# Kernel tuning notes

Measured on AMD Instinct MI355X. Metric: run time of the kernel, lower is better.

Reference implementation:

```python
import jax, jax.numpy as jnp
import numpy as np

B, M, N = 16, 128, 256
USER_DIM, ANT_DIM, EDGE_DIM = 8, 2, 1
HIDDEN, HEADS = 128, 4
HD = HIDDEN // HEADS
WB, DMIN, HZ, PMAX = 2.0, 0.01, 10.0, 1.0
SCALE = 1.0 / float(np.sqrt(HD))
NEG = 0.2  # leaky relu slope


def leaky(x):
    return jnp.where(x >= 0, x, NEG * x)


def ln(x, g, b, eps=1e-5):
    m = jnp.mean(x, axis=-1, keepdims=True)
    v = jnp.mean((x - m) ** 2, axis=-1, keepdims=True)
    return (x - m) * jax.lax.rsqrt(v + eps) * g + b


def setup_inputs() -> dict:
    key = jax.random.key(0)
    ks = jax.random.split(key, 16)
    rn = lambda k, shape, s: jax.random.normal(k, shape, jnp.float32) * s
    inp = {
        "user_feats": jax.random.normal(ks[0], (B, M, USER_DIM), jnp.float32),
        "ant_feats": jax.random.uniform(ks[1], (B, N, ANT_DIM), jnp.float32),
        "edge_feats": jax.random.uniform(ks[2], (B, M, N, EDGE_DIM), jnp.float32),
        # per-head projections (Linear no-bias) + their LayerNorm affine params
        "Wu": rn(ks[3], (HEADS, HD, USER_DIM), 0.5),
        "ln_u_g": jnp.ones((HEADS, HD)), "ln_u_b": jnp.zeros((HEADS, HD)),
        "Wa": rn(ks[4], (HEADS, HD, ANT_DIM), 0.5),
        "ln_a_g": jnp.ones((HEADS, HD)), "ln_a_b": jnp.zeros((HEADS, HD)),
        "We": rn(ks[5], (HEADS, HD, EDGE_DIM), 0.5),
        "ln_e_g": jnp.ones((HEADS, HD)), "ln_e_b": jnp.zeros((HEADS, HD)),
        "attn_v": rn(ks[6], (HEADS, HD), 0.5),
        # residual proj for antennas (the user residual branch is dead code in the block)
        "Wra": rn(ks[7], (HIDDEN, ANT_DIM), 0.5), "bra": jnp.zeros((HIDDEN,)),
        "ln_ant_g": jnp.ones((HIDDEN,)), "ln_ant_b": jnp.zeros((HIDDEN,)),
        # mlp_ant
        "Wm1": rn(ks[8], (HIDDEN // 2, HIDDEN), 0.1), "bm1": jnp.full((HIDDEN // 2,), 0.1),
        "Wm2": rn(ks[9], (2, HIDDEN // 2), 0.1), "bm2": jnp.full((2,), 0.1),
        # readouts over antenna axis
        "Wd1": rn(ks[10], (2 * N, N), 0.05), "bd1": jnp.zeros((2 * N,)),
        "Wd2": rn(ks[11], (N, 2 * N), 0.05), "bd2": jnp.zeros((N,)),
        "Wp1": rn(ks[12], (2 * N, N), 0.05), "bp1": jnp.zeros((2 * N,)),
        "Wp2": rn(ks[13], (N, 2 * N), 0.05), "bp2": jnp.zeros((N,)),
    }
    return inp


def reference(user_feats, ant_feats, edge_feats, Wu, ln_u_g, ln_u_b, Wa, ln_a_g, ln_a_b,
              We, ln_e_g, ln_e_b, attn_v, Wra, bra, ln_ant_g, ln_ant_b,
              Wm1, bm1, Wm2, bm2, Wd1, bd1, Wd2, bd2, Wp1, bp1, Wp2, bp2):
    # --- per-head bipartite attention (all heads batched on axis h) ---
    U = leaky(ln(jnp.einsum('bmi,hdi->hbmd', user_feats, Wu), ln_u_g[:, None, None, :], ln_u_b[:, None, None, :]))  # [h,B,M,hd]
    A = leaky(ln(jnp.einsum('bni,hdi->hbnd', ant_feats, Wa), ln_a_g[:, None, None, :], ln_a_b[:, None, None, :]))   # [h,B,N,hd]
    E = leaky(ln(jnp.einsum('bmni,hdi->hbmnd', edge_feats, We), ln_e_g[:, None, None, None, :], ln_e_b[:, None, None, None, :]))  # [h,B,M,N,hd]
    inter = leaky(U[:, :, :, None, :] + A[:, :, None, :, :] + E)                # [h,B,M,N,hd]
    scores = jnp.einsum('hbmnd,hd->hbmn', inter, attn_v) * SCALE
    alpha = jax.nn.softmax(scores, axis=-1)                                      # max-subtract softmax over N
    ant_out = jnp.einsum('hbmd,hbmn->hbnd', U, alpha)                            # [h,B,N,hd]
    ant_cat = jnp.transpose(ant_out, (1, 2, 0, 3)).reshape(B, N, HIDDEN)         # concat heads
    a_attn = jax.nn.relu(ant_cat + leaky(ant_feats @ Wra.T + bra))
    # --- block readouts ---
    a_attn = ln(a_attn, ln_ant_g, ln_ant_b)
    h1 = jax.nn.relu(a_attn @ Wm1.T + bm1)
    ant2d = jnp.clip(jax.nn.relu(h1 @ Wm2.T + bm2), -200.0, 200.0)               # [B,N,2]
    rd = jax.nn.relu(ant2d[..., 0] @ Wd1.T + bd1) @ Wd2.T + bd2                  # [B,N]
    rp = jax.nn.relu(ant2d[..., 1] @ Wp1.T + bp1) @ Wp2.T + bp2                  # [B,N]
    rd = jnp.clip(rd, 0.0, 100.0)
    rp = jnp.nan_to_num(rp, nan=0.0, posinf=1.0, neginf=0.0)
    # delta path
    Bmax = 2.0 * WB - (N - 1) * DMIN
    da = jax.nn.relu(rd)
    sd = jnp.sum(da, axis=1, keepdims=True)
    sdelta = jnp.clip((Bmax / jnp.maximum(Bmax, sd)) * da, 0.0, 100.0)
    idx = jnp.arange(N, dtype=sdelta.dtype)
    # closed form of the sequential recurrence x[n] = x[n-1] + sdelta[n] + DMIN - WB
    x = jnp.cumsum(sdelta, axis=1) + idx * DMIN - (idx + 1.0) * WB
    positions = jnp.stack([x, jnp.zeros_like(x), jnp.full_like(x, HZ)], axis=-1)  # [B,N,3]
    # power path
    eps = 1e-3
    pa = jnp.clip(jnp.nan_to_num(jax.nn.relu(rp), nan=0.0, posinf=1.0, neginf=0.0), 0.0, 1.0)
    sp = jnp.nan_to_num(jnp.sum(pa, axis=1, keepdims=True), nan=eps, posinf=eps, neginf=-eps)
    denom = jnp.maximum(sp, eps)
    sfp = jax.lax.stop_gradient(jnp.nan_to_num(PMAX / denom, nan=1.0, posinf=1.0, neginf=0.0))
    spow = jnp.clip(jnp.nan_to_num(sfp * pa, nan=0.0, posinf=1.0, neginf=0.0), 0.0, 1.0)
    ant_feats_out = jnp.stack([sdelta, spow], axis=-1)                            # [B,N,2]
    diff = user_feats[..., :2][:, :, None, :] - positions[:, None, :, :2]         # [B,M,N,2]
    edge_feats_new = jnp.sqrt(jnp.sum(diff * diff, axis=-1, keepdims=True))       # [B,M,N,1]
    return (ant_feats_out, edge_feats_new, positions)
```

## Files before the change

### kernel.cpp

```cpp
#include <hip/hip_runtime.h>
#include <math.h>

#define H_   4
#define HD_  32
#define B_   16
#define M_   128
#define N_   256
#define MC_  8
#define MCH_ 16
#define SCALE_ 0.17677669529663687f

__device__ __forceinline__ float lrelu_f(float x) { return x >= 0.f ? x : 0.2f * x; }

__global__ __launch_bounds__(256) void k2_attn(
    const float* __restrict__ uf, const float* __restrict__ af,
    const float* __restrict__ edge,
    const float* __restrict__ Wu, const float* __restrict__ gu, const float* __restrict__ bu,
    const float* __restrict__ Wa, const float* __restrict__ ga, const float* __restrict__ ba,
    const float* __restrict__ We, const float* __restrict__ ge, const float* __restrict__ be,
    const float* __restrict__ av, float* __restrict__ P)
{
  int blk = blockIdx.x;
  int h = blk & 3, b = (blk >> 2) & 15, mc = blk >> 6;
  int tid = threadIdx.x, n = tid;
  int lane = tid & 63, wid = tid >> 6;
  __shared__ float AB[N_ * 33];
  __shared__ float4 Ut4[HD_][4];
  __shared__ float4 cbv[HD_];
  __shared__ float wred[2][MCH_][4];
  __shared__ float vw_s;

  if (tid < 32) {
    int d = tid;
    float w = We[h * HD_ + d];
    float s = w;
    #pragma unroll
    for (int o = 16; o > 0; o >>= 1) s += __shfl_xor(s, o, 32);
    float mw = s * (1.f / 32.f);
    float df = w - mw;
    float v2 = df * df;
    #pragma unroll
    for (int o = 16; o > 0; o >>= 1) v2 += __shfl_xor(v2, o, 32);
    if (d == 0) vw_s = v2 * (1.f / 32.f);
    float vv = av[h * HD_ + d] * SCALE_;
    cbv[d] = make_float4(df * ge[h * HD_ + d], be[h * HD_ + d], 0.6f * vv, 0.4f * vv);
  }
  int m0 = mc * MCH_;
  {
    int m_loc = tid >> 4, s = tid & 15, dd = s * 2;
    const float* urow = uf + (size_t)(b * M_ + m0 + m_loc) * 8;
    const float* w0 = Wu + (h * HD_ + dd) * 8;
    float x0 = 0.f, x1 = 0.f;
    #pragma unroll
    for (int i = 0; i < 8; ++i) { float u = urow[i]; x0 = fmaf(u, w0[i], x0); x1 = fmaf(u, w0[8 + i], x1); }
    float sm = x0 + x1;
    #pragma unroll
    for (int o = 8; o > 0; o >>= 1) sm += __shfl_xor(sm, o, 64);
    float mean = sm * (1.f / 32.f);
    float d0 = x0 - mean, d1 = x1 - mean;
    float vv = fmaf(d0, d0, d1 * d1);
    #pragma unroll
    for (int o = 8; o > 0; o >>= 1) vv += __shfl_xor(vv, o, 64);
    float rs = rsqrtf(vv * (1.f / 32.f) + 1e-5f);
    float y0 = fmaf(d0 * rs, gu[h * HD_ + dd],     bu[h * HD_ + dd]);
    float y1 = fmaf(d1 * rs, gu[h * HD_ + dd + 1], bu[h * HD_ + dd + 1]);
    ((float*)Ut4)[dd * 16 + m_loc]       = lrelu_f(y0);
    ((float*)Ut4)[(dd + 1) * 16 + m_loc] = lrelu_f(y1);
  }
  {
    float a0 = af[(b * N_ + n) * 2 + 0], a1 = af[(b * N_ + n) * 2 + 1];
    float ar[HD_]; float sm = 0.f;
    #pragma unroll
    for (int d = 0; d < HD_; ++d) {
      ar[d] = fmaf(a0, Wa[(h * HD_ + d) * 2], a1 * Wa[(h * HD_ + d) * 2 + 1]);
      sm += ar[d];
    }
    float mean = sm * (1.f / 32.f); float vv = 0.f;
    #pragma unroll
    for (int d = 0; d < HD_; ++d) { ar[d] -= mean; vv = fmaf(ar[d], ar[d], vv); }
    float rs = rsqrtf(vv * (1.f / 32.f) + 1e-5f);
    #pragma unroll
    for (int d = 0; d < HD_; ++d)
      AB[n * 33 + d] = lrelu_f(fmaf(ar[d] * rs, ga[h * HD_ + d], ba[h * HD_ + d]));
  }
  __syncthreads();
  float vw = vw_s;
  float tm[MCH_];
  #pragma unroll
  for (int mm = 0; mm < MCH_; ++mm) {
    float e = edge[(size_t)(b * M_ + m0 + mm) * N_ + n];
    tm[mm] = e * rsqrtf(fmaf(e * e, vw, 1e-5f));
  }
  float sc[MCH_];
  #pragma unroll
  for (int mm = 0; mm < MCH_; ++mm) sc[mm] = 0.f;
  const float* arow = &AB[n * 33];
  for (int d = 0; d < HD_; ++d) {
    float ad = arow[d];
    float4 qc = cbv[d];
    float4 u0 = Ut4[d][0], u1 = Ut4[d][1], u2 = Ut4[d][2], u3 = Ut4[d][3];
#define STEP(mi, uval) { float w_ = fmaf(tm[mi], qc.x, qc.y); \
    float E_ = fmaf(0.4f, fabsf(w_), 0.6f * w_); \
    float x_ = ad + uval + E_; \
    sc[mi] = fmaf(qc.z, x_, fmaf(qc.w, fabsf(x_), sc[mi])); }
    STEP(0, u0.x)  STEP(1, u0.y)  STEP(2, u0.z)  STEP(3, u0.w)
    STEP(4, u1.x)  STEP(5, u1.y)  STEP(6, u1.z)  STEP(7, u1.w)
    STEP(8, u2.x)  STEP(9, u2.y)  STEP(10, u2.z) STEP(11, u2.w)
    STEP(12, u3.x) STEP(13, u3.y) STEP(14, u3.z) STEP(15, u3.w)
#undef STEP
  }
  #pragma unroll
  for (int mm = 0; mm < MCH_; ++mm) {
    float v = sc[mm];
    #pragma unroll
    for (int o = 32; o > 0; o >>= 1) v = fmaxf(v, __shfl_xor(v, o, 64));
    if (lane == 0) wred[0][mm][wid] = v;
  }
  __syncthreads();
  #pragma unroll
  for (int mm = 0; mm < MCH_; ++mm) {
    float mx = fmaxf(fmaxf(wred[0][mm][0], wred[0][mm][1]),
                     fmaxf(wred[0][mm][2], wred[0][mm][3]));
    float em = __expf(sc[mm] - mx);
    sc[mm] = em;
    float ss = em;
    #pragma unroll
    for (int o = 32; o > 0; o >>= 1) ss += __shfl_xor(ss, o, 64);
    if (lane == 0) wred[1][mm][wid] = ss;
  }
  __syncthreads();
  #pragma unroll
  for (int mm = 0; mm < MCH_; ++mm) {
    float tot = (wred[1][mm][0] + wred[1][mm][1]) + (wred[1][mm][2] + wred[1][mm][3]);
    sc[mm] = sc[mm] / tot;
  }
  __syncthreads();
  float* accr = &AB[n * 33];
  for (int d = 0; d < HD_; ++d) {
    float4 u0 = Ut4[d][0], u1 = Ut4[d][1], u2 = Ut4[d][2], u3 = Ut4[d][3];
    float a0 = 0.f;
    a0 = fmaf(sc[0], u0.x, a0);  a0 = fmaf(sc[1], u0.y, a0);
    a0 = fmaf(sc[2], u0.z, a0);  a0 = fmaf(sc[3], u0.w, a0);
    a0 = fmaf(sc[4], u1.x, a0);  a0 = fmaf(sc[5], u1.y, a0);
    a0 = fmaf(sc[6], u1.z, a0);  a0 = fmaf(sc[7], u1.w, a0);
    a0 = fmaf(sc[8], u2.x, a0);  a0 = fmaf(sc[9], u2.y, a0);
    a0 = fmaf(sc[10], u2.z, a0); a0 = fmaf(sc[11], u2.w, a0);
    a0 = fmaf(sc[12], u3.x, a0); a0 = fmaf(sc[13], u3.y, a0);
    a0 = fmaf(sc[14], u3.z, a0); a0 = fmaf(sc[15], u3.w, a0);
    accr[d] = a0;
  }
  __syncthreads();
  float* Pbase = P + (size_t)((mc * 4 + h) * B_ + b) * (N_ * HD_);
  for (int i = tid; i < N_ * HD_; i += 256) {
    int nn = i >> 5, d = i & 31;
    Pbase[i] = AB[nn * 33 + d];
  }
}

__global__ __launch_bounds__(256) void k3_mlp(
    const float* __restrict__ P, const float* __restrict__ af,
    const float* __restrict__ Wra, const float* __restrict__ bra,
    const float* __restrict__ gant, const float* __restrict__ bant,
    const float* __restrict__ Wm1, const float* __restrict__ bm1,
    const float* __restrict__ Wm2, const float* __restrict__ bm2,
    float* __restrict__ rd_in, float* __restrict__ rp_in)
{
  int b = blockIdx.x >> 4, nt = blockIdx.x & 15;
  int tid = threadIdx.x;
  int n_loc = tid >> 4, s = tid & 15;
  int n = nt * 16 + n_loc;
  int jj0 = s * 8;
  int hh = s >> 2, d0 = (s & 3) * 8;
  __shared__ float Wm1s[64][128];
  __shared__ float a2s[16][128];
  __shared__ float h1s[16][64];

  {
    const float4* wg = (const float4*)Wm1;
    float4* wl = (float4*)Wm1s;
    #pragma unroll
    for (int k = 0; k < 8; ++k) wl[tid + 256 * k] = wg[tid + 256 * k];
  }
  float cat[8];
  #pragma unroll
  for (int k = 0; k < 8; ++k) cat[k] = 0.f;
  #pragma unroll
  for (int mc = 0; mc < MC_; ++mc) {
    const float* base = P + (size_t)((mc * 4 + hh) * B_ + b) * (N_ * HD_) + n * HD_ + d0;
    float4 p0 = ((const float4*)base)[0], p1 = ((const float4*)base)[1];
    cat[0] += p0.x; cat[1] += p0.y; cat[2] += p0.z; cat[3] += p0.w;
    cat[4] += p1.x; cat[5] += p1.y; cat[6] += p1.z; cat[7] += p1.w;
  }
  float af0 = af[(b * N_ + n) * 2 + 0], af1 = af[(b * N_ + n) * 2 + 1];
  float a1[8]; float sm = 0.f;
  #pragma unroll
  for (int k = 0; k < 8; ++k) {
    int jj = jj0 + k;
    float r = fmaf(Wra[jj * 2], af0, fmaf(Wra[jj * 2 + 1], af1, bra[jj]));
    a1[k] = fmaxf(cat[k] + lrelu_f(r), 0.f);
    sm += a1[k];
  }
  #pragma unroll
  for (int o = 8; o > 0; o >>= 1) sm += __shfl_xor(sm, o, 64);
  float mean = sm * (1.f / 128.f);
  float vv = 0.f;
  #pragma unroll
  for (int k = 0; k < 8; ++k) { a1[k] -= mean; vv = fmaf(a1[k], a1[k], vv); }
  #pragma unroll
  for (int o = 8; o > 0; o >>= 1) vv += __shfl_xor(vv, o, 64);
  float rs = rsqrtf(vv * (1.f / 128.f) + 1e-5f);
  #pragma unroll
  for (int k = 0; k < 8; ++k) {
    int jj = jj0 + k;
    a2s[n_loc][jj] = fmaf(a1[k] * rs, gant[jj], bant[jj]);
  }
  __syncthreads();
  #pragma unroll
  for (int k = 0; k < 4; ++k) {
    int o = tid + 256 * k;
    int row = o & 63, nl = o >> 6;
    const float4* wr = (const float4*)Wm1s[row];
    const float4* xr = (const float4*)a2s[nl];
    float c0 = 0.f, c1 = 0.f, c2 = 0.f, c3 = 0.f;
    #pragma unroll
    for (int c = 0; c < 32; ++c) {
      int cc = (c + row) & 31;
      float4 w = wr[cc], x = xr[cc];
      c0 = fmaf(w.x, x.x, c0); c1 = fmaf(w.y, x.y, c1);
      c2 = fmaf(w.z, x.z, c2); c3 = fmaf(w.w, x.w, c3);
    }
    h1s[nl][row] = fmaxf((c0 + c1) + (c2 + c3) + bm1[row], 0.f);
  }
  __syncthreads();
  {
    int c = s >> 3, e0 = (s & 7) * 8;
    float p = 0.f;
    #pragma unroll
    for (int k = 0; k < 8; ++k) p = fmaf(h1s[n_loc][e0 + k], Wm2[c * 64 + e0 + k], p);
    #pragma unroll
    for (int o = 4; o > 0; o >>= 1) p += __shfl_xor(p, o, 64);
    if ((s & 7) == 0) {
      float v = p + bm2[c];
      v = fminf(fmaxf(v, 0.f), 200.f);
      (c == 0 ? rd_in : rp_in)[b * N_ + n] = v;
    }
  }
}

__global__ __launch_bounds__(256) void k4a_l1(
    const float* __restrict__ rd_in, const float* __restrict__ rp_in,
    const float* __restrict__ Wd1, const float* __restrict__ bd1,
    const float* __restrict__ Wp1, const float* __restrict__ bp1,
    float* __restrict__ d1buf)
{
  int r = blockIdx.x * 4 + (threadIdx.x >> 6);
  int lane = threadIdx.x & 63;
  int path = r >> 13;
  int rem = r & 8191;
  int b = rem >> 9, i = rem & 511;
  const float* W = (path ? Wp1 : Wd1) + (size_t)i * N_;
  const float* bias = path ? bp1 : bd1;
  const float* x = (path ? rp_in : rd_in) + b * N_;
  float4 w = ((const float4*)W)[lane];
  float4 xv = ((const float4*)x)[lane];
  float s = fmaf(w.x, xv.x, fmaf(w.y, xv.y, fmaf(w.z, xv.z, w.w * xv.w)));
  #pragma unroll
  for (int o = 32; o > 0; o >>= 1) s += __shfl_xor(s, o, 64);
  if (lane == 0) d1buf[r] = fmaxf(s + bias[i], 0.f);
}

__global__ __launch_bounds__(256) void k4b_l2(
    const float* __restrict__ d1buf,
    const float* __restrict__ Wd2, const float* __restrict__ bd2,
    const float* __restrict__ Wp2, const float* __restrict__ bp2,
    float* __restrict__ rdbuf, float* __restrict__ rpbuf)
{
  int r = blockIdx.x * 4 + (threadIdx.x >> 6);
  int lane = threadIdx.x & 63;
  int path = r >> 12;
  int rem = r & 4095;
  int b = rem >> 8, n = rem & 255;
  const float* W = (path ? Wp2 : Wd2) + (size_t)n * (2 * N_);
  const float* x = d1buf + path * (B_ * 2 * N_) + b * (2 * N_);
  float4 w0 = ((const float4*)W)[lane * 2], w1 = ((const float4*)W)[lane * 2 + 1];
  float4 x0 = ((const float4*)x)[lane * 2], x1 = ((const float4*)x)[lane * 2 + 1];
  float s = fmaf(w0.x, x0.x, fmaf(w0.y, x0.y, fmaf(w0.z, x0.z, w0.w * x0.w)));
  s = fmaf(w1.x, x1.x, fmaf(w1.y, x1.y, fmaf(w1.z, x1.z, fmaf(w1.w, x1.w, s))));
  #pragma unroll
  for (int o = 32; o > 0; o >>= 1) s += __shfl_xor(s, o, 64);
  if (lane == 0) {
    if (path == 0) {
      float rd = s + bd2[n];
      rd = fminf(fmaxf(rd, 0.f), 100.f);
      rdbuf[b * N_ + n] = rd;
    } else {
      float rp = s + bp2[n];
      if (isnan(rp)) rp = 0.f;
      else if (isinf(rp)) rp = rp > 0.f ? 1.f : 0.f;
      float pa = fminf(fmaxf(rp, 0.f), 1.f);
      rpbuf[b * N_ + n] = pa;
    }
  }
}

__global__ __launch_bounds__(256) void k4c_final(
    const float* __restrict__ rdbuf, const float* __restrict__ rpbuf,
    const float* __restrict__ uf,
    float* __restrict__ out_af, float* __restrict__ out_pos, float* __restrict__ out_edge)
{
  int b = blockIdx.x >> 4, g = blockIdx.x & 15;
  int q = threadIdx.x;
  int lane = q & 63, wid = q >> 6;
  __shared__ float red[8];
  float rd = rdbuf[b * N_ + q];
  float pa = rpbuf[b * N_ + q];
  float s = rd, s2 = pa;
  #pragma unroll
  for (int o = 32; o > 0; o >>= 1) { s += __shfl_xor(s, o, 64); s2 += __shfl_xor(s2, o, 64); }
  if (lane == 0) { red[wid] = s; red[4 + wid] = s2; }
  __syncthreads();
  float sd = red[0] + red[1] + red[2] + red[3];
  float sp = red[4] + red[5] + red[6] + red[7];
  const float Bmax = 2.f * 2.0f - (N_ - 1) * 0.01f;
  float f = Bmax / fmaxf(Bmax, sd);
  float sdelta = fminf(fmaxf(f * rd, 0.f), 100.f);
  float sfp = 1.0f / fmaxf(sp, 1e-3f);
  float spow = fminf(sfp * pa, 1.f);
  float val = sdelta;
  #pragma unroll
  for (int o = 1; o < 64; o <<= 1) {
    float t = __shfl_up(val, o, 64);
    if (lane >= o) val += t;
  }
  __syncthreads();
  if (lane == 63) red[wid] = val;
  __syncthreads();
  float off = 0.f;
  #pragma unroll
  for (int w2 = 0; w2 < 4; ++w2) if (w2 < wid) off += red[w2];
  float x = val + off + (float)q * 0.01f - (float)(q + 1) * 2.0f;
  if (g == 0) {
    out_af[(b * N_ + q) * 2 + 0] = sdelta;
    out_af[(b * N_ + q) * 2 + 1] = spow;
    out_pos[(b * N_ + q) * 3 + 0] = x;
    out_pos[(b * N_ + q) * 3 + 1] = 0.f;
    out_pos[(b * N_ + q) * 3 + 2] = 10.0f;
  }
  #pragma unroll
  for (int k = 0; k < 8; ++k) {
    int m = g * 8 + k;
    float u0 = uf[(b * M_ + m) * 8 + 0], u1 = uf[(b * M_ + m) * 8 + 1];
    float dx = u0 - x;
    out_edge[(size_t)(b * M_ + m) * N_ + q] = sqrtf(fmaf(dx, dx, u1 * u1));
  }
}

extern "C" void kernel_launch(void* const* d_in, const int* in_sizes, int n_in,
                              void* d_out, int out_size, void* d_ws, size_t ws_size,
                              hipStream_t stream) {
  (void)in_sizes; (void)n_in; (void)out_size; (void)ws_size;
  const float* uf   = (const float*)d_in[0];
  const float* af   = (const float*)d_in[1];
  const float* edge = (const float*)d_in[2];
  const float* Wu   = (const float*)d_in[3];
  const float* gu   = (const float*)d_in[4];
  const float* bu   = (const float*)d_in[5];
  const float* Wa   = (const float*)d_in[6];
  const float* ga   = (const float*)d_in[7];
  const float* ba   = (const float*)d_in[8];
  const float* We   = (const float*)d_in[9];
  const float* ge   = (const float*)d_in[10];
  const float* be   = (const float*)d_in[11];
  const float* av   = (const float*)d_in[12];
  const float* Wra  = (const float*)d_in[13];
  const float* bra  = (const float*)d_in[14];
  const float* gant = (const float*)d_in[15];
  const float* bant = (const float*)d_in[16];
  const float* Wm1  = (const float*)d_in[17];
  const float* bm1  = (const float*)d_in[18];
  const float* Wm2  = (const float*)d_in[19];
  const float* bm2  = (const float*)d_in[20];
  const float* Wd1  = (const float*)d_in[21];
  const float* bd1  = (const float*)d_in[22];
  const float* Wd2  = (const float*)d_in[23];
  const float* bd2  = (const float*)d_in[24];
  const float* Wp1  = (const float*)d_in[25];
  const float* bp1  = (const float*)d_in[26];
  const float* Wp2  = (const float*)d_in[27];
  const float* bp2  = (const float*)d_in[28];

  float* ws    = (float*)d_ws;
  float* P     = ws;
  float* rd_in = ws + 4194304;
  float* rp_in = ws + 4198400;
  float* d1buf = ws + 4202496;
  float* rdbuf = ws + 4218880;
  float* rpbuf = ws + 4222976;

  float* out      = (float*)d_out;
  float* out_af   = out;
  float* out_edge = out + 8192;
  float* out_pos  = out + 532480;

  hipLaunchKernelGGL(k2_attn, dim3(512), dim3(256), 0, stream,
                     uf, af, edge, Wu, gu, bu, Wa, ga, ba, We, ge, be, av, P);
  hipLaunchKernelGGL(k3_mlp, dim3(256), dim3(256), 0, stream,
                     P, af, Wra, bra, gant, bant, Wm1, bm1, Wm2, bm2, rd_in, rp_in);
  hipLaunchKernelGGL(k4a_l1, dim3(4096), dim3(256), 0, stream,
                     rd_in, rp_in, Wd1, bd1, Wp1, bp1, d1buf);
  hipLaunchKernelGGL(k4b_l2, dim3(2048), dim3(256), 0, stream,
                     d1buf, Wd2, bd2, Wp2, bp2, rdbuf, rpbuf);
  hipLaunchKernelGGL(k4c_final, dim3(256), dim3(256), 0, stream,
                     rdbuf, rpbuf, uf, out_af, out_pos, out_edge);
}
```

Measured before the change: 167.8 us.

## Split attention into 16 user chunks and keep antenna features in registers

Halves the per-block user chunk from 16 to 8 and doubles the attention grid to 1024 blocks. The launch bound now asks for 4 blocks per CU, aiming for more waves in flight. Each thread's antenna feature vector stays in registers instead of a shared-memory row, which removes one barrier. The cost is twice as many partial-output tiles, so the P workspace doubles and the MLP kernel must read and reduce twice as many partials.

```diff
diff --git a/kernel.cpp b/kernel.cpp
--- a/kernel.cpp
+++ b/kernel.cpp
@@ -6,13 +6,13 @@
 #define B_   16
 #define M_   128
 #define N_   256
-#define MC_  8
-#define MCH_ 16
+#define MC_  16
+#define MCH_ 8
 #define SCALE_ 0.17677669529663687f
 
 __device__ __forceinline__ float lrelu_f(float x) { return x >= 0.f ? x : 0.2f * x; }
 
-__global__ __launch_bounds__(256) void k2_attn(
+__global__ __launch_bounds__(256, 4) void k2_attn(
     const float* __restrict__ uf, const float* __restrict__ af,
     const float* __restrict__ edge,
     const float* __restrict__ Wu, const float* __restrict__ gu, const float* __restrict__ bu,
@@ -25,7 +25,7 @@
   int tid = threadIdx.x, n = tid;
   int lane = tid & 63, wid = tid >> 6;
   __shared__ float AB[N_ * 33];
-  __shared__ float4 Ut4[HD_][4];
+  __shared__ float4 Ut4[HD_][2];
   __shared__ float4 cbv[HD_];
   __shared__ float wred[2][MCH_][4];
   __shared__ float vw_s;
@@ -46,7 +46,7 @@
     cbv[d] = make_float4(df * ge[h * HD_ + d], be[h * HD_ + d], 0.6f * vv, 0.4f * vv);
   }
   int m0 = mc * MCH_;
-  {
+  if (tid < 128) {
     int m_loc = tid >> 4, s = tid & 15, dd = s * 2;
     const float* urow = uf + (size_t)(b * M_ + m0 + m_loc) * 8;
     const float* w0 = Wu + (h * HD_ + dd) * 8;
@@ -64,12 +64,13 @@
     float rs = rsqrtf(vv * (1.f / 32.f) + 1e-5f);
     float y0 = fmaf(d0 * rs, gu[h * HD_ + dd],     bu[h * HD_ + dd]);
     float y1 = fmaf(d1 * rs, gu[h * HD_ + dd + 1], bu[h * HD_ + dd + 1]);
-    ((float*)Ut4)[dd * 16 + m_loc]       = lrelu_f(y0);
-    ((float*)Ut4)[(dd + 1) * 16 + m_loc] = lrelu_f(y1);
-  }
+    ((float*)Ut4)[dd * MCH_ + m_loc]       = lrelu_f(y0);
+    ((float*)Ut4)[(dd + 1) * MCH_ + m_loc] = lrelu_f(y1);
+  }
+  float ar[HD_];
   {
     float a0 = af[(b * N_ + n) * 2 + 0], a1 = af[(b * N_ + n) * 2 + 1];
-    float ar[HD_]; float sm = 0.f;
+    float sm = 0.f;
     #pragma unroll
     for (int d = 0; d < HD_; ++d) {
       ar[d] = fmaf(a0, Wa[(h * HD_ + d) * 2], a1 * Wa[(h * HD_ + d) * 2 + 1]);
@@ -81,7 +82,7 @@
     float rs = rsqrtf(vv * (1.f / 32.f) + 1e-5f);
     #pragma unroll
     for (int d = 0; d < HD_; ++d)
-      AB[n * 33 + d] = lrelu_f(fmaf(ar[d] * rs, ga[h * HD_ + d], ba[h * HD_ + d]));
+      ar[d] = lrelu_f(fmaf(ar[d] * rs, ga[h * HD_ + d], ba[h * HD_ + d]));
   }
   __syncthreads();
   float vw = vw_s;
@@ -94,19 +95,17 @@
   float sc[MCH_];
   #pragma unroll
   for (int mm = 0; mm < MCH_; ++mm) sc[mm] = 0.f;
-  const float* arow = &AB[n * 33];
+  #pragma unroll
   for (int d = 0; d < HD_; ++d) {
-    float ad = arow[d];
+    float ad = ar[d];
     float4 qc = cbv[d];
-    float4 u0 = Ut4[d][0], u1 = Ut4[d][1], u2 = Ut4[d][2], u3 = Ut4[d][3];
+    float4 u0 = Ut4[d][0], u1 = Ut4[d][1];
 #define STEP(mi, uval) { float w_ = fmaf(tm[mi], qc.x, qc.y); \
     float E_ = fmaf(0.4f, fabsf(w_), 0.6f * w_); \
     float x_ = ad + uval + E_; \
     sc[mi] = fmaf(qc.z, x_, fmaf(qc.w, fabsf(x_), sc[mi])); }
     STEP(0, u0.x)  STEP(1, u0.y)  STEP(2, u0.z)  STEP(3, u0.w)
     STEP(4, u1.x)  STEP(5, u1.y)  STEP(6, u1.z)  STEP(7, u1.w)
-    STEP(8, u2.x)  STEP(9, u2.y)  STEP(10, u2.z) STEP(11, u2.w)
-    STEP(12, u3.x) STEP(13, u3.y) STEP(14, u3.z) STEP(15, u3.w)
 #undef STEP
   }
   #pragma unroll
@@ -134,20 +133,15 @@
     float tot = (wred[1][mm][0] + wred[1][mm][1]) + (wred[1][mm][2] + wred[1][mm][3]);
     sc[mm] = sc[mm] / tot;
   }
-  __syncthreads();
-  float* accr = &AB[n * 33];
+  #pragma unroll
   for (int d = 0; d < HD_; ++d) {
-    float4 u0 = Ut4[d][0], u1 = Ut4[d][1], u2 = Ut4[d][2], u3 = Ut4[d][3];
+    float4 u0 = Ut4[d][0], u1 = Ut4[d][1];
     float a0 = 0.f;
     a0 = fmaf(sc[0], u0.x, a0);  a0 = fmaf(sc[1], u0.y, a0);
     a0 = fmaf(sc[2], u0.z, a0);  a0 = fmaf(sc[3], u0.w, a0);
     a0 = fmaf(sc[4], u1.x, a0);  a0 = fmaf(sc[5], u1.y, a0);
     a0 = fmaf(sc[6], u1.z, a0);  a0 = fmaf(sc[7], u1.w, a0);
-    a0 = fmaf(sc[8], u2.x, a0);  a0 = fmaf(sc[9], u2.y, a0);
-    a0 = fmaf(sc[10], u2.z, a0); a0 = fmaf(sc[11], u2.w, a0);
-    a0 = fmaf(sc[12], u3.x, a0); a0 = fmaf(sc[13], u3.y, a0);
-    a0 = fmaf(sc[14], u3.z, a0); a0 = fmaf(sc[15], u3.w, a0);
-    accr[d] = a0;
+    AB[n * 33 + d] = a0;
   }
   __syncthreads();
   float* Pbase = P + (size_t)((mc * 4 + h) * B_ + b) * (N_ * HD_);
@@ -391,18 +385,18 @@
 
   float* ws    = (float*)d_ws;
   float* P     = ws;
-  float* rd_in = ws + 4194304;
-  float* rp_in = ws + 4198400;
-  float* d1buf = ws + 4202496;
-  float* rdbuf = ws + 4218880;
-  float* rpbuf = ws + 4222976;
+  float* rd_in = ws + 8388608;
+  float* rp_in = ws + 8392704;
+  float* d1buf = ws + 8396800;
+  float* rdbuf = ws + 8413184;
+  float* rpbuf = ws + 8417280;
 
   float* out      = (float*)d_out;
   float* out_af   = out;
   float* out_edge = out + 8192;
   float* out_pos  = out + 532480;
 
-  hipLaunchKernelGGL(k2_attn, dim3(512), dim3(256), 0, stream,
+  hipLaunchKernelGGL(k2_attn, dim3(1024), dim3(256), 0, stream,
                      uf, af, edge, Wu, gu, bu, Wa, ga, ba, We, ge, be, av, P);
   hipLaunchKernelGGL(k3_mlp, dim3(256), dim3(256), 0, stream,
                      P, af, Wra, bra, gant, bant, Wm1, bm1, Wm2, bm2, rd_in, rp_in);
```

New measurement: 471.9 us. 2.81x slower.
